# Optimization experiments

Hardware: AMD Instinct MI355X
Metric: run time of the kernel (lower is better)

Reference implementation:

```python
import jax, jax.numpy as jnp
import numpy as np

N = 10000       # nodes
E = 320000      # edges
D = 256         # feature dim (out_channels)
L = 5           # num_layers


def setup_inputs() -> dict:
    key = jax.random.key(0)
    ks = jax.random.split(key, 8)
    x = jax.random.normal(ks[0], (N, D), dtype=jnp.float32)
    edge_index = jax.random.randint(ks[1], (2, E), 0, N, dtype=jnp.int64)
    edge_attr = jax.random.uniform(ks[2], (E,), dtype=jnp.float32)
    s = 1.0 / np.sqrt(D)
    # per-layer message transform weights [L, D, D]
    weight = jax.random.uniform(ks[3], (L, D, D), minval=-s, maxval=s, dtype=jnp.float32)
    # GRUCell parameters (torch layout: [3D, D] rows = r, z, n)
    w_ih = jax.random.uniform(ks[4], (3 * D, D), minval=-s, maxval=s, dtype=jnp.float32)
    w_hh = jax.random.uniform(ks[5], (3 * D, D), minval=-s, maxval=s, dtype=jnp.float32)
    b_ih = jax.random.uniform(ks[6], (3 * D,), minval=-s, maxval=s, dtype=jnp.float32)
    b_hh = jax.random.uniform(ks[7], (3 * D,), minval=-s, maxval=s, dtype=jnp.float32)
    return {"x": x, "edge_index": edge_index, "edge_attr": edge_attr,
            "weight": weight, "w_ih": w_ih, "w_hh": w_hh,
            "b_ih": b_ih, "b_hh": b_hh}


def _gru_cell(inp, h, w_ih, w_hh, b_ih, b_hh):
    # torch.nn.GRUCell math
    gi = inp @ w_ih.T + b_ih    # [N, 3D]
    gh = h @ w_hh.T + b_hh      # [N, 3D]
    i_r, i_z, i_n = jnp.split(gi, 3, axis=-1)
    h_r, h_z, h_n = jnp.split(gh, 3, axis=-1)
    r = jax.nn.sigmoid(i_r + h_r)
    z = jax.nn.sigmoid(i_z + h_z)
    n = jnp.tanh(i_n + r * h_n)
    return (1.0 - z) * n + z * h


def reference(x, edge_index, edge_attr, weight, w_ih, w_hh, b_ih, b_hh):
    src, dst = edge_index[0], edge_index[1]
    h = x
    for l in range(L):
        m = h @ weight[l]                                   # [N, D]
        msg = m[src] * edge_attr[:, None]                   # [E, D]
        agg = jax.ops.segment_sum(msg, dst, num_segments=N)  # [N, D]
        h = _gru_cell(agg, h, w_ih, w_hh, b_ih, b_hh)
    return h
```

## Files before the change

### kernel.cpp

```cpp
#include <hip/hip_runtime.h>
#include <hip/hip_bf16.h>

#define NN 10000
#define NPAD 10048
#define EE 320000
#define DD 256
#define LL 5

typedef __bf16 bf16x8 __attribute__((ext_vector_type(8)));
typedef __bf16 bf16x4 __attribute__((ext_vector_type(4)));
typedef float f32x4 __attribute__((ext_vector_type(4)));

__device__ __forceinline__ void gload_lds16(const void* g, void* l) {
    __builtin_amdgcn_global_load_lds(
        (const __attribute__((address_space(1))) void*)g,
        (__attribute__((address_space(3))) void*)l, 16, 0, 0);
}


__global__ void prep_k(const float* __restrict__ w_hh, const float* __restrict__ x,
                       __bf16* __restrict__ whhb,
                       float* __restrict__ hb, __bf16* __restrict__ hbfA,
                       __bf16* __restrict__ hbfB, __bf16* __restrict__ aggb,
                       int* __restrict__ deg) {
    int i = blockIdx.x * blockDim.x + threadIdx.x;
    if (i < NN * DD) { float v = x[i]; hb[i] = v; hbfA[i] = (__bf16)v; }
    if (i < 768 * 256) whhb[i] = (__bf16)w_hh[i];
    if (i < (NPAD - NN) * DD) {
        hbfA[NN * DD + i] = (__bf16)0.f;
        hbfB[NN * DD + i] = (__bf16)0.f;
        aggb[NN * DD + i] = (__bf16)0.f;
    }
    if (i < NN) deg[i] = 0;
}

__global__ void hist_k(const int* __restrict__ dst, int* __restrict__ deg) {
    int e = blockIdx.x * blockDim.x + threadIdx.x;
    if (e < EE) atomicAdd(&deg[dst[e]], 1);
}

__global__ void scan_k(const int* __restrict__ deg, int* __restrict__ row_start,
                       int* __restrict__ cursor) {
    __shared__ int sums[1024];
    const int CH = 10;
    int t = threadIdx.x;
    int base = t * CH;
    int loc[CH];
    int s = 0;
#pragma unroll
    for (int i = 0; i < CH; i++) {
        int v = (base + i < NN) ? deg[base + i] : 0;
        loc[i] = s;
        s += v;
    }
    sums[t] = s;
    __syncthreads();
    for (int off = 1; off < 1024; off <<= 1) {
        int v = (t >= off) ? sums[t - off] : 0;
        __syncthreads();
        sums[t] += v;
        __syncthreads();
    }
    int pre = (t == 0) ? 0 : sums[t - 1];
#pragma unroll
    for (int i = 0; i < CH; i++) {
        int idx = base + i;
        if (idx < NN) {
            int v = pre + loc[i];
            row_start[idx] = v;
            cursor[idx] = v;
        }
    }
    if (t == 1023) row_start[NN] = sums[1023];
}

__global__ void fill_k(const int* __restrict__ ei, const float* __restrict__ attr,
                       int* __restrict__ cursor, int* __restrict__ ssrc,
                       float* __restrict__ sattr) {
    int e = blockIdx.x * blockDim.x + threadIdx.x;
    if (e < EE) {
        int dv = ei[EE + e];
        int p = atomicAdd(&cursor[dv], 1);
        ssrc[p] = ei[e];
        sattr[p] = attr[e];
    }
}


__global__ __launch_bounds__(256)
void beff32_k(const float* __restrict__ wih, const float* __restrict__ W,
              __bf16* __restrict__ beff) {
    __shared__ float As[16][68];
    __shared__ float Bs[16][68];
    int l = blockIdx.z;
    const float* Wl = W + (size_t)l * DD * DD;
    __bf16* Cl = beff + (size_t)l * 768 * DD;
    int tid = threadIdx.x;
    int tx = tid & 15, ty = tid >> 4;
    int jBase = blockIdx.x * 64;
    int tBase = blockIdx.y * 64;
    int lr = tid >> 2, lq = tid & 3;
    float acc[4][4];
#pragma unroll
    for (int i = 0; i < 4; i++)
#pragma unroll
        for (int j = 0; j < 4; j++) acc[i][j] = 0.f;

    for (int k0 = 0; k0 < DD; k0 += 16) {
        float4 av = *(const float4*)(wih + (size_t)(jBase + lr) * DD + k0 + lq * 4);
        float4 bv = *(const float4*)(Wl + (size_t)(tBase + lr) * DD + k0 + lq * 4);
        __syncthreads();
        As[lq * 4 + 0][lr] = av.x; As[lq * 4 + 1][lr] = av.y;
        As[lq * 4 + 2][lr] = av.z; As[lq * 4 + 3][lr] = av.w;
        Bs[lq * 4 + 0][lr] = bv.x; Bs[lq * 4 + 1][lr] = bv.y;
        Bs[lq * 4 + 2][lr] = bv.z; Bs[lq * 4 + 3][lr] = bv.w;
        __syncthreads();
#pragma unroll
        for (int kk = 0; kk < 16; kk++) {
            float a0 = As[kk][ty * 4 + 0], a1 = As[kk][ty * 4 + 1];
            float a2 = As[kk][ty * 4 + 2], a3 = As[kk][ty * 4 + 3];
            float b0 = Bs[kk][tx * 4 + 0], b1 = Bs[kk][tx * 4 + 1];
            float b2 = Bs[kk][tx * 4 + 2], b3 = Bs[kk][tx * 4 + 3];
            acc[0][0] += a0 * b0; acc[0][1] += a0 * b1; acc[0][2] += a0 * b2; acc[0][3] += a0 * b3;
            acc[1][0] += a1 * b0; acc[1][1] += a1 * b1; acc[1][2] += a1 * b2; acc[1][3] += a1 * b3;
            acc[2][0] += a2 * b0; acc[2][1] += a2 * b1; acc[2][2] += a2 * b2; acc[2][3] += a2 * b3;
            acc[3][0] += a3 * b0; acc[3][1] += a3 * b1; acc[3][2] += a3 * b2; acc[3][3] += a3 * b3;
        }
    }
#pragma unroll
    for (int i = 0; i < 4; i++) {
        int j = jBase + ty * 4 + i;
        bf16x4 o;
        o[0] = (__bf16)acc[i][0]; o[1] = (__bf16)acc[i][1];
        o[2] = (__bf16)acc[i][2]; o[3] = (__bf16)acc[i][3];
        *(bf16x4*)(Cl + (size_t)j * DD + tBase + tx * 4) = o;
    }
}


__global__ __launch_bounds__(256)
void aggregate_bf_k(const __bf16* __restrict__ hsrc, const int* __restrict__ row_start,
                    const int* __restrict__ ssrc, const float* __restrict__ sattr,
                    __bf16* __restrict__ aggb) {
    __shared__ int sIdx[4][64];
    __shared__ float sAtt[4][64];
    int w = threadIdx.x >> 6, lane = threadIdx.x & 63;
    int n = blockIdx.x * 4 + w;
    int s0 = row_start[n], s1 = row_start[n + 1];
    int half = lane >> 5;
    int c8 = (lane & 31) * 8;

    float acc[8] = {0.f, 0.f, 0.f, 0.f, 0.f, 0.f, 0.f, 0.f};

    for (int base = s0; base < s1; base += 64) {
        int cnt = min(64, s1 - base);
        if (lane < cnt) {
            sIdx[w][lane] = ssrc[base + lane];
            sAtt[w][lane] = sattr[base + lane];
        }
        int t = 0;
        for (; t + 8 <= cnt; t += 8) {
#pragma unroll
            for (int u = 0; u < 4; u++) {
                int e = t + u * 2 + half;
                int s = sIdx[w][e];
                float ww = sAtt[w][e];
                bf16x8 v = *(const bf16x8*)(hsrc + (size_t)s * DD + c8);
#pragma unroll
                for (int i = 0; i < 8; i++) acc[i] += (float)v[i] * ww;
            }
        }
        for (; t + 2 <= cnt; t += 2) {
            int e = t + half;
            int s = sIdx[w][e];
            float ww = sAtt[w][e];
            bf16x8 v = *(const bf16x8*)(hsrc + (size_t)s * DD + c8);
#pragma unroll
            for (int i = 0; i < 8; i++) acc[i] += (float)v[i] * ww;
        }
        if (t < cnt && half == 0) {
            int s = sIdx[w][t];
            float ww = sAtt[w][t];
            bf16x8 v = *(const bf16x8*)(hsrc + (size_t)s * DD + c8);
#pragma unroll
            for (int i = 0; i < 8; i++) acc[i] += (float)v[i] * ww;
        }
    }

#pragma unroll
    for (int i = 0; i < 8; i++) acc[i] += __shfl_xor(acc[i], 32, 64);

    if (half == 0) {
        bf16x8 o;
#pragma unroll
        for (int i = 0; i < 8; i++) o[i] = (__bf16)acc[i];
        *(bf16x8*)(aggb + (size_t)n * DD + c8) = o;
    }
}


__global__ __launch_bounds__(256, 2)
void gru_mfma_k(const __bf16* __restrict__ aggb, const __bf16* __restrict__ hbf,
                const float* __restrict__ hin,
                const __bf16* __restrict__ bihw, const __bf16* __restrict__ whh,
                const float* __restrict__ b_ih, const float* __restrict__ b_hh,
                float* __restrict__ hout, __bf16* __restrict__ hbfout) {
    __shared__ __bf16 sA[2][64][32];
    __shared__ __bf16 sB[6][64][32];
    int tid = threadIdx.x;
    int wave = tid >> 6, lane = tid & 63;
    int ln = lane & 15, quad = lane >> 4;
    int nodeBlock = blockIdx.x * 64;
    int colBlock = blockIdx.y * 64;
    int nodeHalf = (wave >> 1) * 32;
    int colHalf = (wave & 1) * 32;
    int r4 = lane >> 2;
    int kb = (lane & 3) * 8;

    f32x4 acc[6][2][2] = {};

    for (int k0 = 0; k0 < DD; k0 += 32) {
        __syncthreads();
#pragma unroll
        for (int ii = 0; ii < 8; ii++) {
            int idx = wave * 8 + ii;
            const __bf16* src;
            __bf16* dst;
            if (idx < 8) {
                int s = idx >> 2;
                int rg = idx & 3;
                const __bf16* A = s ? hbf : aggb;
                src = A + (size_t)(nodeBlock + rg * 16 + r4) * DD + k0 + kb;
                dst = &sA[s][rg * 16][0];
            } else {
                int j = idx - 8;
                int g6 = j >> 2;
                int rg = j & 3;
                const __bf16* B = (g6 < 3) ? bihw : whh;
                int brow = (g6 % 3) * 256 + colBlock + rg * 16 + r4;
                src = B + (size_t)brow * DD + k0 + kb;
                dst = &sB[g6][rg * 16][0];
            }
            gload_lds16(src, dst);
        }
        __syncthreads();

        bf16x8 aA[2], aH[2];
#pragma unroll
        for (int nf = 0; nf < 2; nf++) {
            aA[nf] = *(const bf16x8*)&sA[0][nodeHalf + nf * 16 + ln][quad * 8];
            aH[nf] = *(const bf16x8*)&sA[1][nodeHalf + nf * 16 + ln][quad * 8];
        }
#pragma unroll
        for (int g = 0; g < 3; g++) {
#pragma unroll
            for (int cc = 0; cc < 2; cc++) {
                bf16x8 bI = *(const bf16x8*)&sB[g][colHalf + cc * 16 + ln][quad * 8];
                bf16x8 bH = *(const bf16x8*)&sB[3 + g][colHalf + cc * 16 + ln][quad * 8];
#pragma unroll
                for (int nf = 0; nf < 2; nf++) {
                    acc[g][nf][cc] = __builtin_amdgcn_mfma_f32_16x16x32_bf16(aA[nf], bI, acc[g][nf][cc], 0, 0, 0);
                    acc[3 + g][nf][cc] = __builtin_amdgcn_mfma_f32_16x16x32_bf16(aH[nf], bH, acc[3 + g][nf][cc], 0, 0, 0);
                }
            }
        }
    }

#pragma unroll
    for (int nf = 0; nf < 2; nf++) {
#pragma unroll
        for (int r = 0; r < 4; r++) {
            int n = nodeBlock + nodeHalf + nf * 16 + quad * 4 + r;
            if (n >= NN) continue;
#pragma unroll
            for (int cc = 0; cc < 2; cc++) {
                int d = colBlock + colHalf + cc * 16 + ln;
                float ir = acc[0][nf][cc][r] + b_ih[d];
                float iz = acc[1][nf][cc][r] + b_ih[d + 256];
                float in_ = acc[2][nf][cc][r] + b_ih[d + 512];
                float hr = acc[3][nf][cc][r] + b_hh[d];
                float hz = acc[4][nf][cc][r] + b_hh[d + 256];
                float hn = acc[5][nf][cc][r] + b_hh[d + 512];
                float rr = 1.f / (1.f + __expf(-(ir + hr)));
                float zz = 1.f / (1.f + __expf(-(iz + hz)));
                float ax = in_ + rr * hn;
                float e2 = __expf(-2.f * ax);
                float nnv = 2.f / (1.f + e2) - 1.f;
                float hp = hin[(size_t)n * DD + d];
                float o = (1.f - zz) * nnv + zz * hp;
                hout[(size_t)n * DD + d] = o;
                hbfout[(size_t)n * DD + d] = (__bf16)o;
            }
        }
    }
}


extern "C" void kernel_launch(void* const* d_in, const int* in_sizes, int n_in,
                              void* d_out, int out_size, void* d_ws, size_t ws_size,
                              hipStream_t stream) {
    const float* x = (const float*)d_in[0];
    const int* edge_index = (const int*)d_in[1];
    const float* edge_attr = (const float*)d_in[2];
    const float* weight = (const float*)d_in[3];
    const float* w_ih = (const float*)d_in[4];
    const float* w_hh = (const float*)d_in[5];
    const float* b_ih = (const float*)d_in[6];
    const float* b_hh = (const float*)d_in[7];

    size_t off = 0;
    char* base = (char*)d_ws;
    auto carve = [&](size_t bytes) -> void* {
        void* p = base + off;
        off += (bytes + 255) & ~(size_t)255;
        return p;
    };
    float* hb = (float*)carve((size_t)NPAD * DD * 4);
    __bf16* hbfA = (__bf16*)carve((size_t)NPAD * DD * 2);
    __bf16* hbfB = (__bf16*)carve((size_t)NPAD * DD * 2);
    __bf16* aggb = (__bf16*)carve((size_t)NPAD * DD * 2);
    __bf16* whhb = (__bf16*)carve((size_t)768 * DD * 2);
    __bf16* beff = (__bf16*)carve((size_t)LL * 768 * DD * 2);
    int* deg = (int*)carve((size_t)NN * 4);
    int* row_start = (int*)carve((size_t)(NN + 1) * 4);
    int* cursor = (int*)carve((size_t)NN * 4);
    int* ssrc = (int*)carve((size_t)EE * 4);
    float* sattr = (float*)carve((size_t)EE * 4);
    (void)ws_size;

    prep_k<<<(NN * DD + 255) / 256, 256, 0, stream>>>(w_hh, x, whhb, hb, hbfA, hbfB,
                                                      aggb, deg);
    hist_k<<<(EE + 255) / 256, 256, 0, stream>>>(edge_index + EE, deg);
    scan_k<<<1, 1024, 0, stream>>>(deg, row_start, cursor);
    fill_k<<<(EE + 255) / 256, 256, 0, stream>>>(edge_index, edge_attr, cursor, ssrc, sattr);
    beff32_k<<<dim3(12, 4, LL), 256, 0, stream>>>(w_ih, weight, beff);

    float* hA = hb;
    float* hB = (float*)d_out;
    __bf16* hbfIn = hbfA;
    __bf16* hbfOut = hbfB;
    for (int l = 0; l < LL; l++) {
        aggregate_bf_k<<<2500, 256, 0, stream>>>(hbfIn, row_start, ssrc, sattr, aggb);
        gru_mfma_k<<<dim3(157, 4), 256, 0, stream>>>(aggb, hbfIn, hA,
                                                     beff + (size_t)l * 768 * DD, whhb,
                                                     b_ih, b_hh, hB, hbfOut);
        float* t = hA; hA = hB; hB = t;
        __bf16* tb = hbfIn; hbfIn = hbfOut; hbfOut = tb;
    }
}
```

Before: 352.1 us.

## Use 8 waves per GRU block with K=64 staging per barrier

The GRU MFMA kernel moves from 4 to 8 waves per block, so each wave computes a 16-node by 32-column tile and needs half as many accumulators. Each global-to-LDS stage now loads 64 K-elements in two sub-tiles, which halves the number of barrier pairs per K loop. The aim is to cut register pressure, raise the number of waves that can hide latency, and reduce synchronisation. The cost is that each wave reuses its A fragments over fewer MFMAs, so LDS read traffic per MFMA goes up, and shared memory per block doubles.

```diff
diff --git a/kernel.cpp b/kernel.cpp
--- a/kernel.cpp
+++ b/kernel.cpp
@@ -199,98 +199,93 @@
 }
 
 
-__global__ __launch_bounds__(256, 2)
+__global__ __launch_bounds__(512, 2)
 void gru_mfma_k(const __bf16* __restrict__ aggb, const __bf16* __restrict__ hbf,
                 const float* __restrict__ hin,
                 const __bf16* __restrict__ bihw, const __bf16* __restrict__ whh,
                 const float* __restrict__ b_ih, const float* __restrict__ b_hh,
                 float* __restrict__ hout, __bf16* __restrict__ hbfout) {
-    __shared__ __bf16 sA[2][64][32];
-    __shared__ __bf16 sB[6][64][32];
+    __shared__ __bf16 sA[2][2][64][32];
+    __shared__ __bf16 sB[6][2][64][32];
     int tid = threadIdx.x;
     int wave = tid >> 6, lane = tid & 63;
     int ln = lane & 15, quad = lane >> 4;
     int nodeBlock = blockIdx.x * 64;
     int colBlock = blockIdx.y * 64;
-    int nodeHalf = (wave >> 1) * 32;
-    int colHalf = (wave & 1) * 32;
+    int nf = wave & 3;
+    int ch = (wave >> 2) * 32;
     int r4 = lane >> 2;
     int kb = (lane & 3) * 8;
 
-    f32x4 acc[6][2][2] = {};
-
-    for (int k0 = 0; k0 < DD; k0 += 32) {
+    f32x4 acc[6][2] = {};
+
+    for (int k0 = 0; k0 < DD; k0 += 64) {
         __syncthreads();
 #pragma unroll
         for (int ii = 0; ii < 8; ii++) {
             int idx = wave * 8 + ii;
             const __bf16* src;
             __bf16* dst;
-            if (idx < 8) {
-                int s = idx >> 2;
+            if (idx < 16) {
+                int mat = idx >> 3;
+                int ksub = (idx >> 2) & 1;
                 int rg = idx & 3;
-                const __bf16* A = s ? hbf : aggb;
-                src = A + (size_t)(nodeBlock + rg * 16 + r4) * DD + k0 + kb;
-                dst = &sA[s][rg * 16][0];
+                const __bf16* A = mat ? hbf : aggb;
+                src = A + (size_t)(nodeBlock + rg * 16 + r4) * DD + k0 + ksub * 32 + kb;
+                dst = &sA[mat][ksub][rg * 16][0];
             } else {
-                int j = idx - 8;
-                int g6 = j >> 2;
+                int j = idx - 16;
+                int g6 = j >> 3;
+                int ksub = (j >> 2) & 1;
                 int rg = j & 3;
                 const __bf16* B = (g6 < 3) ? bihw : whh;
                 int brow = (g6 % 3) * 256 + colBlock + rg * 16 + r4;
-                src = B + (size_t)brow * DD + k0 + kb;
-                dst = &sB[g6][rg * 16][0];
+                src = B + (size_t)brow * DD + k0 + ksub * 32 + kb;
+                dst = &sB[g6][ksub][rg * 16][0];
             }
             gload_lds16(src, dst);
         }
         __syncthreads();
 
-        bf16x8 aA[2], aH[2];
-#pragma unroll
-        for (int nf = 0; nf < 2; nf++) {
-            aA[nf] = *(const bf16x8*)&sA[0][nodeHalf + nf * 16 + ln][quad * 8];
-            aH[nf] = *(const bf16x8*)&sA[1][nodeHalf + nf * 16 + ln][quad * 8];
-        }
-#pragma unroll
-        for (int g = 0; g < 3; g++) {
-#pragma unroll
-            for (int cc = 0; cc < 2; cc++) {
-                bf16x8 bI = *(const bf16x8*)&sB[g][colHalf + cc * 16 + ln][quad * 8];
-                bf16x8 bH = *(const bf16x8*)&sB[3 + g][colHalf + cc * 16 + ln][quad * 8];
-#pragma unroll
-                for (int nf = 0; nf < 2; nf++) {
-                    acc[g][nf][cc] = __builtin_amdgcn_mfma_f32_16x16x32_bf16(aA[nf], bI, acc[g][nf][cc], 0, 0, 0);
-                    acc[3 + g][nf][cc] = __builtin_amdgcn_mfma_f32_16x16x32_bf16(aH[nf], bH, acc[3 + g][nf][cc], 0, 0, 0);
+#pragma unroll
+        for (int ksub = 0; ksub < 2; ksub++) {
+            bf16x8 aA = *(const bf16x8*)&sA[0][ksub][nf * 16 + ln][quad * 8];
+            bf16x8 aH = *(const bf16x8*)&sA[1][ksub][nf * 16 + ln][quad * 8];
+#pragma unroll
+            for (int g = 0; g < 3; g++) {
+#pragma unroll
+                for (int cc = 0; cc < 2; cc++) {
+                    bf16x8 bI = *(const bf16x8*)&sB[g][ksub][ch + cc * 16 + ln][quad * 8];
+                    bf16x8 bH = *(const bf16x8*)&sB[3 + g][ksub][ch + cc * 16 + ln][quad * 8];
+                    acc[g][cc] = __builtin_amdgcn_mfma_f32_16x16x32_bf16(aA, bI, acc[g][cc], 0, 0, 0);
+                    acc[3 + g][cc] = __builtin_amdgcn_mfma_f32_16x16x32_bf16(aH, bH, acc[3 + g][cc], 0, 0, 0);
                 }
             }
         }
     }
 
 #pragma unroll
-    for (int nf = 0; nf < 2; nf++) {
-#pragma unroll
-        for (int r = 0; r < 4; r++) {
-            int n = nodeBlock + nodeHalf + nf * 16 + quad * 4 + r;
-            if (n >= NN) continue;
-#pragma unroll
-            for (int cc = 0; cc < 2; cc++) {
-                int d = colBlock + colHalf + cc * 16 + ln;
-                float ir = acc[0][nf][cc][r] + b_ih[d];
-                float iz = acc[1][nf][cc][r] + b_ih[d + 256];
-                float in_ = acc[2][nf][cc][r] + b_ih[d + 512];
-                float hr = acc[3][nf][cc][r] + b_hh[d];
-                float hz = acc[4][nf][cc][r] + b_hh[d + 256];
-                float hn = acc[5][nf][cc][r] + b_hh[d + 512];
-                float rr = 1.f / (1.f + __expf(-(ir + hr)));
-                float zz = 1.f / (1.f + __expf(-(iz + hz)));
-                float ax = in_ + rr * hn;
-                float e2 = __expf(-2.f * ax);
-                float nnv = 2.f / (1.f + e2) - 1.f;
-                float hp = hin[(size_t)n * DD + d];
-                float o = (1.f - zz) * nnv + zz * hp;
-                hout[(size_t)n * DD + d] = o;
-                hbfout[(size_t)n * DD + d] = (__bf16)o;
-            }
+    for (int r = 0; r < 4; r++) {
+        int n = nodeBlock + nf * 16 + quad * 4 + r;
+        if (n >= NN) continue;
+#pragma unroll
+        for (int cc = 0; cc < 2; cc++) {
+            int d = colBlock + ch + cc * 16 + ln;
+            float ir = acc[0][cc][r] + b_ih[d];
+            float iz = acc[1][cc][r] + b_ih[d + 256];
+            float in_ = acc[2][cc][r] + b_ih[d + 512];
+            float hr = acc[3][cc][r] + b_hh[d];
+            float hz = acc[4][cc][r] + b_hh[d + 256];
+            float hn = acc[5][cc][r] + b_hh[d + 512];
+            float rr = 1.f / (1.f + __expf(-(ir + hr)));
+            float zz = 1.f / (1.f + __expf(-(iz + hz)));
+            float ax = in_ + rr * hn;
+            float e2 = __expf(-2.f * ax);
+            float nnv = 2.f / (1.f + e2) - 1.f;
+            float hp = hin[(size_t)n * DD + d];
+            float o = (1.f - zz) * nnv + zz * hp;
+            hout[(size_t)n * DD + d] = o;
+            hbfout[(size_t)n * DD + d] = (__bf16)o;
         }
     }
 }
@@ -341,7 +336,7 @@
     __bf16* hbfOut = hbfB;
     for (int l = 0; l < LL; l++) {
         aggregate_bf_k<<<2500, 256, 0, stream>>>(hbfIn, row_start, ssrc, sattr, aggb);
-        gru_mfma_k<<<dim3(157, 4), 256, 0, stream>>>(aggb, hbfIn, hA,
+        gru_mfma_k<<<dim3(157, 4), 512, 0, stream>>>(aggb, hbfIn, hA,
                                                      beff + (size_t)l * 768 * DD, whhb,
                                                      b_ih, b_hh, hB, hbfOut);
         float* t = hA; hA = hB; hB = t;
```

After: 356.7 us. No clear change (+1.3%).
